# Kernel optimization log

Measured on AMD Instinct MI355X. Metric: run time of the kernel, lower is better.

The kernel has to match this reference:

```python
import jax, jax.numpy as jnp
import numpy as np
from jax import lax

B, H, W, C, NH = 16, 56, 56, 192, 6
L = H * W
DH = C // NH            # 32
HID = 4 * C             # 768
ETA = 1.0 / DH          # TTT inner-loop learning rate
EPS = 1e-5

# ---- RoPE rotation tables (deterministic buffer, shape (H, W, C//2)) ----
_kmax = C // 4
_theta = 1.0 / (10000.0 ** (np.arange(_kmax) / _kmax))
_ii, _jj = np.meshgrid(np.arange(H), np.arange(W), indexing='ij')
_ang = np.concatenate([_ii[..., None] * _theta, _jj[..., None] * _theta], axis=-1)  # (H,W,C/2)
_COS = jnp.asarray(np.cos(_ang), dtype=jnp.float32)
_SIN = jnp.asarray(np.sin(_ang), dtype=jnp.float32)


def layernorm(x, g, b):
    mu = jnp.mean(x, axis=-1, keepdims=True)
    var = jnp.mean(jnp.square(x - mu), axis=-1, keepdims=True)
    return (x - mu) * lax.rsqrt(var + EPS) * g + b


def dwconv3x3(x_blc, w, b):
    # x: (B, L, Ch) -> depthwise 3x3 conv over (H, W) -> (B, L, Ch)
    Ch = x_blc.shape[-1]
    xi = x_blc.reshape(B, H, W, Ch).transpose(0, 3, 1, 2)  # NCHW
    y = lax.conv_general_dilated(xi, w, (1, 1), 'SAME', feature_group_count=Ch,
                                 dimension_numbers=('NCHW', 'OIHW', 'NCHW'))
    y = y + b[None, :, None, None]
    return y.transpose(0, 2, 3, 1).reshape(B, L, Ch)


def rope(x):
    # x: (B, L, C); rotate complex pairs with 2D axial angles
    xr = x.reshape(B, H, W, C // 2, 2)
    re, im = xr[..., 0], xr[..., 1]
    o_re = _COS * re - _SIN * im
    o_im = _SIN * re + _COS * im
    return jnp.stack([o_re, o_im], axis=-1).reshape(B, L, C)


def ttt_attn(xn, qkv_w, qkv_b, W0, proj_w, proj_b):
    qkv = xn @ qkv_w.T + qkv_b                      # (B, L, 3C)
    q, k, v = jnp.split(qkv, 3, axis=-1)
    q = rope(q) * (DH ** -0.5)
    k = rope(k)

    def to_heads(t):  # (B,L,C) -> (L, B*NH, DH)
        return t.reshape(B, L, NH, DH).transpose(1, 0, 2, 3).reshape(L, B * NH, DH)
    qs, ks, vs = to_heads(q), to_heads(k), to_heads(v)

    Wst0 = jnp.broadcast_to(W0[None], (B, NH, DH, DH)).reshape(B * NH, DH, DH)

    def step(Wst, qkv_t):
        qt, kt, vt = qkv_t
        pred = jnp.einsum('bij,bj->bi', Wst, kt)
        Wn = Wst - ETA * (pred - vt)[:, :, None] * kt[:, None, :]
        ot = jnp.einsum('bij,bj->bi', Wn, qt)
        return Wn, ot

    _, out = lax.scan(step, Wst0, (qs, ks, vs))     # out: (L, B*NH, DH)
    out = out.reshape(L, B, NH, DH).transpose(1, 0, 2, 3).reshape(B, L, C)
    return out @ proj_w.T + proj_b


def setup_inputs() -> dict:
    key = jax.random.key(0)
    ks = jax.random.split(key, 12)
    s = 0.02
    return {
        'x': jax.random.normal(ks[0], (B, L, C), jnp.float32),
        'cpe_w': jax.random.normal(ks[1], (C, 1, 3, 3), jnp.float32) * s,
        'cpe_b': jnp.zeros((C,), jnp.float32),
        'n1_g': jnp.ones((C,), jnp.float32),
        'n1_b': jnp.zeros((C,), jnp.float32),
        'qkv_w': jax.random.normal(ks[2], (3 * C, C), jnp.float32) * s,
        'qkv_b': jnp.zeros((3 * C,), jnp.float32),
        'W0': jax.random.normal(ks[3], (NH, DH, DH), jnp.float32) * s,
        'proj_w': jax.random.normal(ks[4], (C, C), jnp.float32) * s,
        'proj_b': jnp.zeros((C,), jnp.float32),
        'n2_g': jnp.ones((C,), jnp.float32),
        'n2_b': jnp.zeros((C,), jnp.float32),
        'fc1_w': jax.random.normal(ks[5], (HID, C), jnp.float32) * s,
        'fc1_b': jnp.zeros((HID,), jnp.float32),
        'dwc_w': jax.random.normal(ks[6], (HID, 1, 3, 3), jnp.float32) * s,
        'dwc_b': jnp.zeros((HID,), jnp.float32),
        'fc2_w': jax.random.normal(ks[7], (C, HID), jnp.float32) * s,
        'fc2_b': jnp.zeros((C,), jnp.float32),
    }


def reference(x, cpe_w, cpe_b, n1_g, n1_b, qkv_w, qkv_b, W0, proj_w, proj_b,
              n2_g, n2_b, fc1_w, fc1_b, dwc_w, dwc_b, fc2_w, fc2_b):
    # CPE: conditional positional encoding (depthwise conv residual)
    x = x + dwconv3x3(x, cpe_w, cpe_b)
    # TTT attention branch
    x = x + ttt_attn(layernorm(x, n1_g, n1_b), qkv_w, qkv_b, W0, proj_w, proj_b)
    # MLP branch with depthwise conv
    h1 = jax.nn.gelu(layernorm(x, n2_g, n2_b) @ fc1_w.T + fc1_b, approximate=False)
    h1 = jax.nn.gelu(h1 + dwconv3x3(h1, dwc_w, dwc_b), approximate=False)
    x = x + (h1 @ fc2_w.T + fc2_b)
    return x
```

## Files before the change

### kernel.cpp

```cpp
#include <hip/hip_runtime.h>
#include <hip/hip_bf16.h>

#define Bc 16
#define Hc 56
#define Wcc 56
#define Cc 192
#define NHc 6
#define Lc 3136
#define DHc 32
#define HIDc 768
#define NHEAD 96
#define Sc 32
#define NCHUNK 98
#define NPAIR (NHEAD*NCHUNK)
#define ROWS (Bc*Lc)
#define GR2 (ROWS/2)
#define ETAc (1.0f/32.0f)

typedef unsigned short u16;
typedef unsigned int u32;
typedef __attribute__((ext_vector_type(8))) short bf16x8;
typedef __attribute__((ext_vector_type(4))) float f32x4;
typedef __attribute__((ext_vector_type(16))) float f32x16;

__device__ __forceinline__ float b2f(u16 v){ u32 u = ((u32)v)<<16; float f; __builtin_memcpy(&f,&u,4); return f; }
__device__ __forceinline__ u16 f2b(float f){ u32 u; __builtin_memcpy(&u,&f,4); u32 r = u + 0x7FFFu + ((u>>16)&1u); return (u16)(r>>16); }
__device__ __forceinline__ f32x16 zero16(){ f32x16 z = {0,0,0,0,0,0,0,0,0,0,0,0,0,0,0,0}; return z; }

__device__ __forceinline__ void make_bfrags(const f32x16& t, int hi, bf16x8& b1, bf16x8& b2){
  u32 P[8], S[8];
  #pragma unroll
  for (int q=0;q<4;q++){
    #pragma unroll
    for (int j=0;j<2;j++){
      u32 r; float lo = t[4*q+2*j], hv = t[4*q+2*j+1];
      asm("v_cvt_pk_bf16_f32 %0, %1, %2" : "=v"(r) : "v"(lo), "v"(hv));
      P[2*q+j] = r;
    }
  }
  #pragma unroll
  for (int i=0;i<8;i++) S[i] = (u32)__shfl_xor((int)P[i], 32);
  union { u32 u[4]; bf16x8 v; } f1, f2;
  if (hi==0){ f1.u[0]=P[0]; f1.u[1]=P[1]; f1.u[2]=S[0]; f1.u[3]=S[1];
              f2.u[0]=P[4]; f2.u[1]=P[5]; f2.u[2]=S[4]; f2.u[3]=S[5]; }
  else      { f1.u[0]=S[2]; f1.u[1]=S[3]; f1.u[2]=P[2]; f1.u[3]=P[3];
              f2.u[0]=S[6]; f2.u[1]=S[7]; f2.u[2]=P[6]; f2.u[3]=P[7]; }
  b1 = f1.v; b2 = f2.v;
}

__global__ __launch_bounds__(256) void cast_bf16_kernel(const float* __restrict__ src, u16* __restrict__ dst, int n){
  int i = blockIdx.x*256 + threadIdx.x;
  if (i < n) dst[i] = f2b(src[i]);
}

__global__ __launch_bounds__(256) void dwt_kernel(const float* __restrict__ w, float* __restrict__ wt, int CH){
  int i = blockIdx.x*256 + threadIdx.x;
  if (i < CH*9){ int ch = i/9, t = i - ch*9; wt[t*CH + ch] = w[i]; }
}

__global__ __launch_bounds__(256) void rope_tab_kernel(float* __restrict__ ct, float* __restrict__ st){
  int i = blockIdx.x*256 + threadIdx.x;
  int l = i/96, p = i - l*96;
  int h = l/Wcc, w = l - h*Wcc;
  int kk = (p<48)? p : p-48;
  float th = powf(10000.f, -(float)kk/48.f);
  float ang = (float)((p<48)? h : w) * th;
  ct[i] = cosf(ang);
  st[i] = sinf(ang);
}

__global__ __launch_bounds__(256) void cpe_kernel(const float* __restrict__ x, const float* __restrict__ cwt9,
                                                  const float* __restrict__ bs, u16* __restrict__ x1){
  int gid = blockIdx.x*256 + threadIdx.x;
  int cg = gid % 24; int row = gid / 24; int ch0 = cg*8;
  int l = row % Lc; int h = l/Wcc, w = l - h*Wcc;
  const float* xp = x + (size_t)row*Cc + ch0;
  float acc[8];
  { f32x4 b0 = *(const f32x4*)(bs+ch0), b1v = *(const f32x4*)(bs+ch0+4);
    acc[0]=b0[0];acc[1]=b0[1];acc[2]=b0[2];acc[3]=b0[3];
    acc[4]=b1v[0];acc[5]=b1v[1];acc[6]=b1v[2];acc[7]=b1v[3]; }
  #pragma unroll
  for (int kh=0;kh<3;kh++){
    int hh = h+kh-1; if (hh<0 || hh>=Hc) continue;
    #pragma unroll
    for (int kw=0;kw<3;kw++){
      int ww = w+kw-1; if (ww<0 || ww>=Wcc) continue;
      const float* ip = xp + ((kh-1)*Wcc + (kw-1))*Cc;
      f32x4 i0 = *(const f32x4*)ip, i1 = *(const f32x4*)(ip+4);
      const float* wp = cwt9 + (kh*3+kw)*Cc + ch0;
      f32x4 w0 = *(const f32x4*)wp, w1 = *(const f32x4*)(wp+4);
      acc[0] += i0[0]*w0[0]; acc[1] += i0[1]*w0[1]; acc[2] += i0[2]*w0[2]; acc[3] += i0[3]*w0[3];
      acc[4] += i1[0]*w1[0]; acc[5] += i1[1]*w1[1]; acc[6] += i1[2]*w1[2]; acc[7] += i1[3]*w1[3];
    }
  }
  f32x4 c0 = *(const f32x4*)xp, c1 = *(const f32x4*)(xp+4);
  union { bf16x8 v; u16 s[8]; } ov;
  ov.s[0]=f2b(c0[0]+acc[0]); ov.s[1]=f2b(c0[1]+acc[1]); ov.s[2]=f2b(c0[2]+acc[2]); ov.s[3]=f2b(c0[3]+acc[3]);
  ov.s[4]=f2b(c1[0]+acc[4]); ov.s[5]=f2b(c1[1]+acc[5]); ov.s[6]=f2b(c1[2]+acc[6]); ov.s[7]=f2b(c1[3]+acc[7]);
  *(bf16x8*)(x1 + (size_t)row*Cc + ch0) = ov.v;
}

template<int INF32>
__global__ __launch_bounds__(256) void ln_kernel(const u16* __restrict__ xb, const float* __restrict__ xf,
                                                 const float* __restrict__ g, const float* __restrict__ b,
                                                 u16* __restrict__ out){
  int row = blockIdx.x*4 + (threadIdx.x>>6);
  int lane = threadIdx.x & 63;
  float v0, v1, v2;
  if (INF32){
    const float* xr = xf + (size_t)row*Cc;
    v0 = xr[lane]; v1 = xr[lane+64]; v2 = xr[lane+128];
  } else {
    const u16* xr = xb + (size_t)row*Cc;
    v0 = b2f(xr[lane]); v1 = b2f(xr[lane+64]); v2 = b2f(xr[lane+128]);
  }
  float s = v0+v1+v2;
  float q = v0*v0 + v1*v1 + v2*v2;
  #pragma unroll
  for (int off=32; off; off>>=1){ s += __shfl_xor(s, off); q += __shfl_xor(q, off); }
  float mu = s*(1.f/Cc);
  float var = q*(1.f/Cc) - mu*mu;
  float rs = rsqrtf(var + 1e-5f);
  u16* orow = out + (size_t)row*Cc;
  orow[lane]     = f2b((v0-mu)*rs*g[lane]     + b[lane]);
  orow[lane+64]  = f2b((v1-mu)*rs*g[lane+64]  + b[lane+64]);
  orow[lane+128] = f2b((v2-mu)*rs*g[lane+128] + b[lane+128]);
}

template<int MODE, int BLKM, int KT>
__global__ __launch_bounds__(256) void gemm_kernel(
    const u16* __restrict__ A, const u16* __restrict__ Wt,
    const float* __restrict__ bias,
    float* __restrict__ outf, u16* __restrict__ outb,
    u16* __restrict__ vdst, const u16* __restrict__ residb, const float* __restrict__ residf)
{
  constexpr int WROWS = BLKM/2;
  constexpr int NF = WROWS/16;
  constexpr int NCH = KT/192;
  constexpr int NG = BLKM*192/(256*8);
  __shared__ u16 As[BLKM*200];
  int tid = threadIdx.x;
  int wid = tid>>6, lane = tid&63;
  int wr = wid>>1, wc = wid&1;
  int m0 = blockIdx.x*BLKM;
  int n0 = blockIdx.y*192 + wc*96;
  int ar = lane&15, kg = lane>>4;
  f32x4 acc[NF][6];
  #pragma unroll
  for (int f=0;f<NF;f++)
    #pragma unroll
    for (int c=0;c<6;c++){ f32x4 z = {0.f,0.f,0.f,0.f}; acc[f][c] = z; }
  bf16x8 bcur[6], bnxt[6];
  #pragma unroll
  for (int c=0;c<6;c++) bcur[c] = *(const bf16x8*)(Wt + (size_t)(n0 + c*16 + ar)*KT + kg*8);
  #pragma unroll
  for (int ch=0; ch<NCH; ch++){
    if (ch>0) __syncthreads();
    #pragma unroll
    for (int j=0;j<NG;j++){
      int g = j*256 + tid;
      int grow = g/24, gcol = (g - grow*24)*8;
      bf16x8 v = *(const bf16x8*)(A + (size_t)(m0+grow)*KT + ch*192 + gcol);
      *(bf16x8*)(As + grow*200 + gcol) = v;
    }
    __syncthreads();
    #pragma unroll
    for (int kc=0;kc<6;kc++){
      int s = ch*6 + kc;
      if (s+1 < NCH*6){
        int koff = ((s+1)/6)*192 + ((s+1)%6)*32 + kg*8;
        #pragma unroll
        for (int c=0;c<6;c++) bnxt[c] = *(const bf16x8*)(Wt + (size_t)(n0 + c*16 + ar)*KT + koff);
      }
      bf16x8 af[NF];
      #pragma unroll
      for (int f=0;f<NF;f++)
        af[f] = *(const bf16x8*)(As + (wr*WROWS + f*16 + ar)*200 + kc*32 + kg*8);
      #pragma unroll
      for (int f=0;f<NF;f++)
        #pragma unroll
        for (int c=0;c<6;c++)
          acc[f][c] = __builtin_amdgcn_mfma_f32_16x16x32_bf16(af[f], bcur[c], acc[f][c], 0,0,0);
      #pragma unroll
      for (int c=0;c<6;c++) bcur[c] = bnxt[c];
    }
  }
  int rb = kg*4;
  #pragma unroll
  for (int f=0;f<NF;f++){
    #pragma unroll
    for (int c=0;c<6;c++){
      int col = n0 + c*16 + ar;
      float bv = bias[col];
      #pragma unroll
      for (int j=0;j<4;j++){
        int row = m0 + wr*WROWS + f*16 + rb + j;
        float v = acc[f][c][j] + bv;
        if (MODE==0){
          if (col < 384) outb[(size_t)row*384 + col] = f2b(v);
          else {
            int bb = row/Lc; int l = row - bb*Lc;
            int nh = (col-384)>>5; int d = col&31;
            vdst[(((size_t)(bb*NHc+nh))*Lc + l)*DHc + d] = f2b(v);
          }
        } else if (MODE==1){
          outf[(size_t)row*Cc + col] = v + b2f(residb[(size_t)row*Cc + col]);
        } else if (MODE==2){
          float gv = 0.5f*v*(1.f + erff(v*0.70710678118654752f));
          outb[(size_t)row*HIDc + col] = f2b(gv);
        } else {
          outf[(size_t)row*Cc + col] = v + residf[(size_t)row*Cc + col];
        }
      }
    }
  }
}

__global__ __launch_bounds__(256) void rope_kernel(const u16* __restrict__ qk, const float* __restrict__ ct,
                                                   const float* __restrict__ st, u16* __restrict__ q_s, u16* __restrict__ k_s){
  int gid = blockIdx.x*256 + threadIdx.x;
  int sub = gid % 24; int row = gid / 24;
  int bb = row / Lc; int l = row - bb*Lc;
  bool isq = sub < 12; int pg = isq ? sub : sub-12;
  int p0 = pg*8;
  int cbase = (isq ? 0 : 192) + 2*p0;
  const u16* qr = qk + (size_t)row*384 + cbase;
  bf16x8 in0 = *(const bf16x8*)qr;
  bf16x8 in1 = *(const bf16x8*)(qr + 8);
  const float* cp = ct + l*96 + p0;
  const float* sp = st + l*96 + p0;
  f32x4 c0 = *(const f32x4*)cp, c1 = *(const f32x4*)(cp+4);
  f32x4 s0 = *(const f32x4*)sp, s1 = *(const f32x4*)(sp+4);
  float cs[8] = {c0[0],c0[1],c0[2],c0[3],c1[0],c1[1],c1[2],c1[3]};
  float sn[8] = {s0[0],s0[1],s0[2],s0[3],s1[0],s1[1],s1[2],s1[3]};
  float sc = isq ? 0.1767766952966369f : 1.0f;
  union { bf16x8 v; u16 s[8]; } o0, o1;
  #pragma unroll
  for (int j=0;j<4;j++){
    float re = b2f((u16)in0[2*j]), im = b2f((u16)in0[2*j+1]);
    o0.s[2*j]   = f2b((cs[j]*re - sn[j]*im)*sc);
    o0.s[2*j+1] = f2b((sn[j]*re + cs[j]*im)*sc);
  }
  #pragma unroll
  for (int j=0;j<4;j++){
    float re = b2f((u16)in1[2*j]), im = b2f((u16)in1[2*j+1]);
    o1.s[2*j]   = f2b((cs[4+j]*re - sn[4+j]*im)*sc);
    o1.s[2*j+1] = f2b((sn[4+j]*re + cs[4+j]*im)*sc);
  }
  int nh = pg>>1, d0 = (pg&1)*16;
  u16* dst = (isq ? q_s : k_s) + (((size_t)(bb*NHc+nh))*Lc + l)*DHc + d0;
  *(bf16x8*)dst = o0.v;
  *(bf16x8*)(dst+8) = o1.v;
}

__global__ __launch_bounds__(64) void ttta_kernel(const u16* __restrict__ k_s, const u16* __restrict__ v_s,
                                                  u16* __restrict__ u_s, u16* __restrict__ rn_s,
                                                  u16* __restrict__ af_s, u16* __restrict__ bc_s){
  __shared__ float Gl[1024];
  __shared__ u16 LK[32*40];
  __shared__ float LU[32*33];
  __shared__ float LR[32*33];
  int pair = blockIdx.x;
  int head = pair / NCHUNK;
  int l0 = (pair - head*NCHUNK) * Sc;
  int lane = threadIdx.x; int rr = lane&31; int hi = lane>>5; int ks = hi*8;
  const u16* kb = k_s + ((size_t)head*Lc + l0)*DHc;
  bf16x8 a0 = *(const bf16x8*)(kb + rr*32 + ks);
  bf16x8 a1 = *(const bf16x8*)(kb + rr*32 + 16 + ks);
  *(bf16x8*)(LK + rr*40 + ks) = a0;
  *(bf16x8*)(LK + rr*40 + 16 + ks) = a1;
  f32x16 g = zero16();
  g = __builtin_amdgcn_mfma_f32_32x32x16_bf16(a0, a0, g, 0,0,0);
  g = __builtin_amdgcn_mfma_f32_32x32x16_bf16(a1, a1, g, 0,0,0);
  #pragma unroll
  for (int reg=0;reg<16;reg++){
    int i = (reg&3) + 8*(reg>>2) + 4*hi;
    Gl[i*32 + rr] = ETAc * g[reg];
  }
  __syncthreads();
  float X[32];
  if (lane < 32){
    #pragma unroll
    for (int i=0;i<32;i++) X[i] = ETAc * b2f(v_s[((size_t)head*Lc + l0 + i)*DHc + lane]);
  } else {
    int m = lane-32;
    #pragma unroll
    for (int i=0;i<32;i++) X[i] = ETAc * b2f(kb[i*32 + m]);
  }
  #pragma unroll
  for (int i=1;i<32;i++){
    float a = X[i];
    #pragma unroll
    for (int j=0;j<i;j++) a -= Gl[i*32+j]*X[j];
    X[i] = a;
  }
  if (lane < 32){
    u16* dst = u_s + (size_t)pair*1024 + lane;
    #pragma unroll
    for (int i=0;i<32;i++) dst[i*32] = f2b(X[i]);
    #pragma unroll
    for (int i=0;i<32;i++) LU[lane*33 + i] = X[i];
  } else {
    u16* dst = rn_s + (size_t)pair*1024 + (lane&31);
    #pragma unroll
    for (int i=0;i<32;i++) dst[i*32] = f2b(-X[i]);
    #pragma unroll
    for (int i=0;i<32;i++) LR[(lane&31)*33 + i] = X[i];
  }
  __syncthreads();
  union { bf16x8 v; u16 s[8]; } kc1, kc2, uc1, uc2, rc1, rc2;
  #pragma unroll
  for (int s=0;s<8;s++){
    kc1.s[s] = LK[(ks+s)*40 + rr];
    kc2.s[s] = LK[(16+ks+s)*40 + rr];
    uc1.s[s] = f2b(LU[rr*33 + ks+s]);
    uc2.s[s] = f2b(LU[rr*33 + 16+ks+s]);
    rc1.s[s] = f2b(LR[rr*33 + ks+s]);
    rc2.s[s] = f2b(LR[rr*33 + 16+ks+s]);
  }
  f32x16 bacc = zero16();
  bacc = __builtin_amdgcn_mfma_f32_32x32x16_bf16(kc1.v, uc1.v, bacc, 0,0,0);
  bacc = __builtin_amdgcn_mfma_f32_32x32x16_bf16(kc2.v, uc2.v, bacc, 0,0,0);
  union { bf16x8 v; u16 s[8]; } bo1, bo2;
  #pragma unroll
  for (int r=0;r<8;r++){ bo1.s[r] = f2b(bacc[r]); bo2.s[r] = f2b(bacc[8+r]); }
  *(bf16x8*)(bc_s + (size_t)pair*1024 + lane*16) = bo1.v;
  *(bf16x8*)(bc_s + (size_t)pair*1024 + lane*16 + 8) = bo2.v;
  f32x16 aacc = zero16();
  aacc = __builtin_amdgcn_mfma_f32_32x32x16_bf16(rc1.v, kc1.v, aacc, 0,0,0);
  aacc = __builtin_amdgcn_mfma_f32_32x32x16_bf16(rc2.v, kc2.v, aacc, 0,0,0);
  f32x16 an;
  #pragma unroll
  for (int r=0;r<16;r++) an[r] = -aacc[r];
  bf16x8 f1, f2;
  make_bfrags(an, hi, f1, f2);
  *(bf16x8*)(af_s + (size_t)pair*1024 + lane*16) = f1;
  *(bf16x8*)(af_s + (size_t)pair*1024 + lane*16 + 8) = f2;
}

__global__ __launch_bounds__(64) void tttb_kernel(const u16* __restrict__ af_s, const u16* __restrict__ bc_s,
                                                  const float* __restrict__ W0, u16* __restrict__ w_snap){
  int head = blockIdx.x; int nh = head % NHc;
  int lane = threadIdx.x; int rr = lane&31; int hi = lane>>5;
  f32x16 T;
  const float* w0r = W0 + nh*1024 + rr*32 + 4*hi;
  #pragma unroll
  for (int q=0;q<4;q++){
    f32x4 v = *(const f32x4*)(w0r + 8*q);
    T[4*q+0]=v[0]; T[4*q+1]=v[1]; T[4*q+2]=v[2]; T[4*q+3]=v[3];
  }
  size_t hb = (size_t)head*NCHUNK;
  const bf16x8* afp = (const bf16x8*)(af_s + hb*1024);
  const bf16x8* bcp = (const bf16x8*)(bc_s + hb*1024);
  bf16x8 A1 = afp[lane*2], A2 = afp[lane*2+1];
  bf16x8 Bv1 = bcp[lane*2], Bv2 = bcp[lane*2+1];
  bf16x8 b1, b2;
  make_bfrags(T, hi, b1, b2);
  for (int c=0;c<NCHUNK;c++){
    bf16x8 nA1=A1, nA2=A2, nB1=Bv1, nB2=Bv2;
    if (c+1 < NCHUNK){
      int base = (c+1)*128 + lane*2;
      nA1 = afp[base]; nA2 = afp[base+1];
      nB1 = bcp[base]; nB2 = bcp[base+1];
    }
    u16* wrow = w_snap + (hb + c)*1024 + rr*32;
    *(bf16x8*)(wrow + hi*8) = b1;
    *(bf16x8*)(wrow + 16 + hi*8) = b2;
    f32x16 acc;
    #pragma unroll
    for (int r=0;r<8;r++){ acc[r] = T[r] + b2f((u16)Bv1[r]); acc[8+r] = T[8+r] + b2f((u16)Bv2[r]); }
    acc = __builtin_amdgcn_mfma_f32_32x32x16_bf16(A1, b1, acc, 0,0,0);
    acc = __builtin_amdgcn_mfma_f32_32x32x16_bf16(A2, b2, acc, 0,0,0);
    T = acc;
    make_bfrags(T, hi, b1, b2);
    A1=nA1; A2=nA2; Bv1=nB1; Bv2=nB2;
  }
}

__global__ __launch_bounds__(64) void tttc_kernel(const u16* __restrict__ q_s, const u16* __restrict__ k_s,
                                                  const u16* __restrict__ w_snap, const u16* __restrict__ u_s,
                                                  const u16* __restrict__ rn_s, u16* __restrict__ o_bf){
  __shared__ __align__(16) u16 Pl[32*40];
  int pair = blockIdx.x;
  int head = pair / NCHUNK;
  int ch = pair - head*NCHUNK;
  int l0 = ch*Sc;
  int lane = threadIdx.x; int rr = lane&31; int hi = lane>>5; int ks = hi*8;
  const u16* qb = q_s + ((size_t)head*Lc + l0)*DHc;
  const u16* kb = k_s + ((size_t)head*Lc + l0)*DHc;
  bf16x8 q0 = *(const bf16x8*)(qb + rr*32 + ks);
  bf16x8 q1 = *(const bf16x8*)(qb + rr*32 + 16 + ks);
  bf16x8 k0 = *(const bf16x8*)(kb + rr*32 + ks);
  bf16x8 k1 = *(const bf16x8*)(kb + rr*32 + 16 + ks);
  f32x16 p = zero16();
  p = __builtin_amdgcn_mfma_f32_32x32x16_bf16(q0, k0, p, 0,0,0);
  p = __builtin_amdgcn_mfma_f32_32x32x16_bf16(q1, k1, p, 0,0,0);
  #pragma unroll
  for (int reg=0;reg<16;reg++){
    int i = (reg&3)+8*(reg>>2)+4*hi;
    Pl[i*40+rr] = (rr<=i) ? f2b(p[reg]) : (u16)0;
  }
  const u16* wsb = w_snap + (size_t)pair*1024;
  bf16x8 tb0 = *(const bf16x8*)(wsb + rr*32 + ks);
  bf16x8 tb1 = *(const bf16x8*)(wsb + rr*32 + 16 + ks);
  const u16* ub = u_s + (size_t)pair*1024;
  f32x16 wr;
  #pragma unroll
  for (int r=0;r<16;r++){
    int i = (r&3)+8*(r>>2)+4*hi;
    wr[r] = b2f(ub[i*32 + rr]);
  }
  const u16* rb = rn_s + (size_t)pair*1024;
  bf16x8 rn0 = *(const bf16x8*)(rb + rr*32 + ks);
  bf16x8 rn1 = *(const bf16x8*)(rb + rr*32 + 16 + ks);
  wr = __builtin_amdgcn_mfma_f32_32x32x16_bf16(rn0, tb0, wr, 0,0,0);
  wr = __builtin_amdgcn_mfma_f32_32x32x16_bf16(rn1, tb1, wr, 0,0,0);
  bf16x8 wb0, wb1;
  make_bfrags(wr, hi, wb0, wb1);
  __syncthreads();
  f32x16 o = zero16();
  o = __builtin_amdgcn_mfma_f32_32x32x16_bf16(q0, tb0, o, 0,0,0);
  o = __builtin_amdgcn_mfma_f32_32x32x16_bf16(q1, tb1, o, 0,0,0);
  bf16x8 pa0 = *(const bf16x8*)(Pl + rr*40 + ks);
  bf16x8 pa1 = *(const bf16x8*)(Pl + rr*40 + 16 + ks);
  o = __builtin_amdgcn_mfma_f32_32x32x16_bf16(pa0, wb0, o, 0,0,0);
  o = __builtin_amdgcn_mfma_f32_32x32x16_bf16(pa1, wb1, o, 0,0,0);
  int bb = head/NHc, nh = head - bb*NHc;
  #pragma unroll
  for (int reg=0;reg<16;reg++){
    int i = (reg&3)+8*(reg>>2)+4*hi;
    o_bf[((size_t)(bb*Lc + l0 + i))*Cc + nh*32 + rr] = f2b(o[reg]);
  }
}

__global__ __launch_bounds__(256) void dwc_kernel(const u16* __restrict__ h1, const float* __restrict__ wt9,
                                                  const float* __restrict__ bs, u16* __restrict__ h2, int row0){
  int gid = blockIdx.x*256 + threadIdx.x;
  int cg = gid % 96; int lrow = gid / 96; int ch0 = cg*8;
  int row = row0 + lrow;
  int l = row % Lc; int h = l/Wcc, w = l - h*Wcc;
  const u16* hp = h1 + (size_t)lrow*HIDc + ch0;
  float acc[8];
  { f32x4 b0 = *(const f32x4*)(bs+ch0), b1v = *(const f32x4*)(bs+ch0+4);
    acc[0]=b0[0];acc[1]=b0[1];acc[2]=b0[2];acc[3]=b0[3];
    acc[4]=b1v[0];acc[5]=b1v[1];acc[6]=b1v[2];acc[7]=b1v[3]; }
  #pragma unroll
  for (int kh=0;kh<3;kh++){
    int hh = h+kh-1; if (hh<0 || hh>=Hc) continue;
    #pragma unroll
    for (int kw=0;kw<3;kw++){
      int ww = w+kw-1; if (ww<0 || ww>=Wcc) continue;
      bf16x8 iv = *(const bf16x8*)(hp + ((kh-1)*Wcc + (kw-1))*HIDc);
      const float* wp = wt9 + (kh*3+kw)*HIDc + ch0;
      f32x4 w0 = *(const f32x4*)wp, w1 = *(const f32x4*)(wp+4);
      acc[0] += b2f((u16)iv[0])*w0[0]; acc[1] += b2f((u16)iv[1])*w0[1];
      acc[2] += b2f((u16)iv[2])*w0[2]; acc[3] += b2f((u16)iv[3])*w0[3];
      acc[4] += b2f((u16)iv[4])*w1[0]; acc[5] += b2f((u16)iv[5])*w1[1];
      acc[6] += b2f((u16)iv[6])*w1[2]; acc[7] += b2f((u16)iv[7])*w1[3];
    }
  }
  bf16x8 cv = *(const bf16x8*)hp;
  union { bf16x8 v; u16 s[8]; } ov;
  #pragma unroll
  for (int j=0;j<8;j++){
    float v = b2f((u16)cv[j]) + acc[j];
    ov.s[j] = f2b(0.5f*v*(1.f + erff(v*0.70710678118654752f)));
  }
  *(bf16x8*)(h2 + (size_t)lrow*HIDc + ch0) = ov.v;
}

extern "C" void kernel_launch(void* const* d_in, const int* in_sizes, int n_in,
                              void* d_out, int out_size, void* d_ws, size_t ws_size,
                              hipStream_t stream){
  const float* x     = (const float*)d_in[0];
  const float* cpe_w = (const float*)d_in[1];
  const float* cpe_b = (const float*)d_in[2];
  const float* n1_g  = (const float*)d_in[3];
  const float* n1_b  = (const float*)d_in[4];
  const float* qkv_w = (const float*)d_in[5];
  const float* qkv_b = (const float*)d_in[6];
  const float* W0    = (const float*)d_in[7];
  const float* proj_w= (const float*)d_in[8];
  const float* proj_b= (const float*)d_in[9];
  const float* n2_g  = (const float*)d_in[10];
  const float* n2_b  = (const float*)d_in[11];
  const float* fc1_w = (const float*)d_in[12];
  const float* fc1_b = (const float*)d_in[13];
  const float* dwc_w = (const float*)d_in[14];
  const float* dwc_b = (const float*)d_in[15];
  const float* fc2_w = (const float*)d_in[16];
  const float* fc2_b = (const float*)d_in[17];

  char* ws = (char*)d_ws;
  size_t off = 0;
  auto alloc = [&](size_t bytes)->char*{
    char* p = ws + off;
    off += (bytes + 255) & ~(size_t)255;
    return p;
  };
  u16* wbqkv = (u16*)alloc((size_t)576*192*2);
  u16* wbproj= (u16*)alloc((size_t)192*192*2);
  u16* wbfc1 = (u16*)alloc((size_t)768*192*2);
  u16* wbfc2 = (u16*)alloc((size_t)192*768*2);
  float* dwt9 = (float*)alloc((size_t)9*HIDc*4);
  float* cwt9 = (float*)alloc((size_t)9*Cc*4);
  float* ctab = (float*)alloc((size_t)Lc*96*4);
  float* stab = (float*)alloc((size_t)Lc*96*4);
  u16* regA = (u16*)alloc((size_t)ROWS*Cc*2);
  u16* regB = (u16*)alloc((size_t)ROWS*Cc*2);
  u16* regD = (u16*)alloc((size_t)NHEAD*Lc*DHc*2);
  u16* regE = (u16*)alloc((size_t)NHEAD*Lc*DHc*2);
  u16* rn_s = (u16*)alloc((size_t)NPAIR*1024*2);
  u16* af_s = (u16*)alloc((size_t)NPAIR*1024*2);
  u16* wsn  = (u16*)alloc((size_t)NPAIR*1024*2);
  u16* qk = (u16*)d_out;
  u16* us = (u16*)d_out;
  u16* bc = us + (size_t)NPAIR*1024;
  float* x2 = (float*)d_out;

  u16* x1 = regA;
  u16* xn = regB;
  u16* qs = regB;
  u16* xn2 = regB;
  u16* vs = regD;
  u16* obf = regD;
  u16* ksb = regE;
  u16* h1 = regD;
  u16* h2 = rn_s;

  cast_bf16_kernel<<<(576*192+255)/256,256,0,stream>>>(qkv_w, wbqkv, 576*192);
  cast_bf16_kernel<<<(192*192+255)/256,256,0,stream>>>(proj_w, wbproj, 192*192);
  cast_bf16_kernel<<<(768*192+255)/256,256,0,stream>>>(fc1_w, wbfc1, 768*192);
  cast_bf16_kernel<<<(192*768+255)/256,256,0,stream>>>(fc2_w, wbfc2, 192*768);
  dwt_kernel<<<(768*9+255)/256,256,0,stream>>>(dwc_w, dwt9, HIDc);
  dwt_kernel<<<(192*9+255)/256,256,0,stream>>>(cpe_w, cwt9, Cc);
  rope_tab_kernel<<<(Lc*96)/256,256,0,stream>>>(ctab, stab);

  cpe_kernel<<<(ROWS*24)/256,256,0,stream>>>(x, cwt9, cpe_b, x1);
  ln_kernel<0><<<ROWS/4,256,0,stream>>>(x1, nullptr, n1_g, n1_b, xn);
  { dim3 g(ROWS/128, 3); gemm_kernel<0,128,192><<<g,256,0,stream>>>(xn, wbqkv, qkv_b, nullptr, qk, vs, nullptr, nullptr); }
  rope_kernel<<<(ROWS*24)/256,256,0,stream>>>(qk, ctab, stab, qs, ksb);
  ttta_kernel<<<NPAIR,64,0,stream>>>(ksb, vs, us, rn_s, af_s, bc);
  tttb_kernel<<<NHEAD,64,0,stream>>>(af_s, bc, W0, wsn);
  tttc_kernel<<<NPAIR,64,0,stream>>>(qs, ksb, wsn, us, rn_s, obf);
  { dim3 g(ROWS/128, 1); gemm_kernel<1,128,192><<<g,256,0,stream>>>(obf, wbproj, proj_b, x2, nullptr, nullptr, x1, nullptr); }
  ln_kernel<1><<<ROWS/4,256,0,stream>>>(nullptr, x2, n2_g, n2_b, xn2);
  for (int g4=0; g4<2; g4++){
    const u16* a_in = xn2 + (size_t)g4*GR2*Cc;
    float* xo = x2 + (size_t)g4*GR2*Cc;
    { dim3 g(GR2/128, 4); gemm_kernel<2,128,192><<<g,256,0,stream>>>(a_in, wbfc1, fc1_b, nullptr, h1, nullptr, nullptr, nullptr); }
    dwc_kernel<<<(GR2*96)/256,256,0,stream>>>(h1, dwt9, dwc_b, h2, g4*GR2);
    { dim3 g(GR2/64, 1); gemm_kernel<3,64,768><<<g,256,0,stream>>>(h2, wbfc2, fc2_b, xo, nullptr, nullptr, nullptr, xo); }
  }
}
```

Baseline: 553.6 us.

## Stage GEMM epilogues through LDS for coalesced vector stores and shrink row tile

```diff
diff --git a/kernel.cpp b/kernel.cpp
--- a/kernel.cpp
+++ b/kernel.cpp
@@ -127,27 +127,28 @@
   orow[lane+128] = f2b((v2-mu)*rs*g[lane+128] + b[lane+128]);
 }
 
-template<int MODE, int BLKM, int KT>
+template<int MODE, int KT>
 __global__ __launch_bounds__(256) void gemm_kernel(
     const u16* __restrict__ A, const u16* __restrict__ Wt,
     const float* __restrict__ bias,
     float* __restrict__ outf, u16* __restrict__ outb,
     u16* __restrict__ vdst, const u16* __restrict__ residb, const float* __restrict__ residf)
 {
-  constexpr int WROWS = BLKM/2;
-  constexpr int NF = WROWS/16;
   constexpr int NCH = KT/192;
-  constexpr int NG = BLKM*192/(256*8);
-  __shared__ u16 As[BLKM*200];
+  __shared__ __align__(16) char smem[64*200*2];
+  u16* As = (u16*)smem;
+  float* Os32 = (float*)smem;
+  u16* Osu = (u16*)smem;
   int tid = threadIdx.x;
   int wid = tid>>6, lane = tid&63;
   int wr = wid>>1, wc = wid&1;
-  int m0 = blockIdx.x*BLKM;
-  int n0 = blockIdx.y*192 + wc*96;
+  int m0 = blockIdx.x*64;
+  int nblk = blockIdx.y*192;
+  int n0 = nblk + wc*96;
   int ar = lane&15, kg = lane>>4;
-  f32x4 acc[NF][6];
-  #pragma unroll
-  for (int f=0;f<NF;f++)
+  f32x4 acc[2][6];
+  #pragma unroll
+  for (int f=0;f<2;f++)
     #pragma unroll
     for (int c=0;c<6;c++){ f32x4 z = {0.f,0.f,0.f,0.f}; acc[f][c] = z; }
   bf16x8 bcur[6], bnxt[6];
@@ -157,7 +158,7 @@
   for (int ch=0; ch<NCH; ch++){
     if (ch>0) __syncthreads();
     #pragma unroll
-    for (int j=0;j<NG;j++){
+    for (int j=0;j<6;j++){
       int g = j*256 + tid;
       int grow = g/24, gcol = (g - grow*24)*8;
       bf16x8 v = *(const bf16x8*)(A + (size_t)(m0+grow)*KT + ch*192 + gcol);
@@ -172,12 +173,12 @@
         #pragma unroll
         for (int c=0;c<6;c++) bnxt[c] = *(const bf16x8*)(Wt + (size_t)(n0 + c*16 + ar)*KT + koff);
       }
-      bf16x8 af[NF];
+      bf16x8 af[2];
       #pragma unroll
-      for (int f=0;f<NF;f++)
-        af[f] = *(const bf16x8*)(As + (wr*WROWS + f*16 + ar)*200 + kc*32 + kg*8);
+      for (int f=0;f<2;f++)
+        af[f] = *(const bf16x8*)(As + (wr*32 + f*16 + ar)*200 + kc*32 + kg*8);
       #pragma unroll
-      for (int f=0;f<NF;f++)
+      for (int f=0;f<2;f++)
         #pragma unroll
         for (int c=0;c<6;c++)
           acc[f][c] = __builtin_amdgcn_mfma_f32_16x16x32_bf16(af[f], bcur[c], acc[f][c], 0,0,0);
@@ -185,33 +186,70 @@
       for (int c=0;c<6;c++) bcur[c] = bnxt[c];
     }
   }
-  int rb = kg*4;
-  #pragma unroll
-  for (int f=0;f<NF;f++){
-    #pragma unroll
-    for (int c=0;c<6;c++){
-      int col = n0 + c*16 + ar;
-      float bv = bias[col];
+  __syncthreads();
+  if (MODE==0 || MODE==2){
+    #pragma unroll
+    for (int f=0;f<2;f++){
       #pragma unroll
-      for (int j=0;j<4;j++){
-        int row = m0 + wr*WROWS + f*16 + rb + j;
-        float v = acc[f][c][j] + bv;
-        if (MODE==0){
-          if (col < 384) outb[(size_t)row*384 + col] = f2b(v);
-          else {
-            int bb = row/Lc; int l = row - bb*Lc;
-            int nh = (col-384)>>5; int d = col&31;
-            vdst[(((size_t)(bb*NHc+nh))*Lc + l)*DHc + d] = f2b(v);
-          }
-        } else if (MODE==1){
-          outf[(size_t)row*Cc + col] = v + b2f(residb[(size_t)row*Cc + col]);
-        } else if (MODE==2){
-          float gv = 0.5f*v*(1.f + erff(v*0.70710678118654752f));
-          outb[(size_t)row*HIDc + col] = f2b(gv);
-        } else {
-          outf[(size_t)row*Cc + col] = v + residf[(size_t)row*Cc + col];
+      for (int c=0;c<6;c++){
+        float bv = bias[n0 + c*16 + ar];
+        #pragma unroll
+        for (int j=0;j<4;j++){
+          float v = acc[f][c][j] + bv;
+          if (MODE==2) v = 0.5f*v*(1.f + erff(v*0.70710678118654752f));
+          Osu[(wr*32 + f*16 + kg*4 + j)*200 + wc*96 + c*16 + ar] = f2b(v);
         }
       }
+    }
+    __syncthreads();
+    #pragma unroll
+    for (int j=0;j<6;j++){
+      int g = j*256 + tid;
+      int grow = g/24, gcol = (g - grow*24)*8;
+      bf16x8 v = *(const bf16x8*)(Osu + grow*200 + gcol);
+      int row = m0 + grow, col = nblk + gcol;
+      if (MODE==2){
+        *(bf16x8*)(outb + (size_t)row*HIDc + col) = v;
+      } else if (col < 384){
+        *(bf16x8*)(outb + (size_t)row*384 + col) = v;
+      } else {
+        int bb = row/Lc; int l = row - bb*Lc;
+        int nh = gcol>>5, d = gcol&31;
+        *(bf16x8*)(vdst + (((size_t)(bb*NHc+nh))*Lc + l)*DHc + d) = v;
+      }
+    }
+  } else {
+    #pragma unroll
+    for (int half=0; half<2; half++){
+      if (wc==half){
+        #pragma unroll
+        for (int f=0;f<2;f++){
+          #pragma unroll
+          for (int c=0;c<6;c++){
+            float bv = bias[n0 + c*16 + ar];
+            #pragma unroll
+            for (int j=0;j<4;j++)
+              Os32[(wr*32 + f*16 + kg*4 + j)*100 + c*16 + ar] = acc[f][c][j] + bv;
+          }
+        }
+      }
+      __syncthreads();
+      #pragma unroll
+      for (int j=0;j<6;j++){
+        int g = j*256 + tid;
+        int grow = g/24, qcol = (g - grow*24)*4;
+        f32x4 v = *(const f32x4*)(Os32 + grow*100 + qcol);
+        int row = m0 + grow, colg = half*96 + qcol;
+        if (MODE==1){
+          const u16* rp = residb + (size_t)row*Cc + colg;
+          v[0] += b2f(rp[0]); v[1] += b2f(rp[1]); v[2] += b2f(rp[2]); v[3] += b2f(rp[3]);
+        } else {
+          f32x4 rv = *(const f32x4*)(residf + (size_t)row*Cc + colg);
+          v[0] += rv[0]; v[1] += rv[1]; v[2] += rv[2]; v[3] += rv[3];
+        }
+        *(f32x4*)(outf + (size_t)row*Cc + colg) = v;
+      }
+      if (half==0) __syncthreads();
     }
   }
 }
@@ -538,18 +576,18 @@
 
   cpe_kernel<<<(ROWS*24)/256,256,0,stream>>>(x, cwt9, cpe_b, x1);
   ln_kernel<0><<<ROWS/4,256,0,stream>>>(x1, nullptr, n1_g, n1_b, xn);
-  { dim3 g(ROWS/128, 3); gemm_kernel<0,128,192><<<g,256,0,stream>>>(xn, wbqkv, qkv_b, nullptr, qk, vs, nullptr, nullptr); }
+  { dim3 g(ROWS/64, 3); gemm_kernel<0,192><<<g,256,0,stream>>>(xn, wbqkv, qkv_b, nullptr, qk, vs, nullptr, nullptr); }
   rope_kernel<<<(ROWS*24)/256,256,0,stream>>>(qk, ctab, stab, qs, ksb);
   ttta_kernel<<<NPAIR,64,0,stream>>>(ksb, vs, us, rn_s, af_s, bc);
   tttb_kernel<<<NHEAD,64,0,stream>>>(af_s, bc, W0, wsn);
   tttc_kernel<<<NPAIR,64,0,stream>>>(qs, ksb, wsn, us, rn_s, obf);
-  { dim3 g(ROWS/128, 1); gemm_kernel<1,128,192><<<g,256,0,stream>>>(obf, wbproj, proj_b, x2, nullptr, nullptr, x1, nullptr); }
+  { dim3 g(ROWS/64, 1); gemm_kernel<1,192><<<g,256,0,stream>>>(obf, wbproj, proj_b, x2, nullptr, nullptr, x1, nullptr); }
   ln_kernel<1><<<ROWS/4,256,0,stream>>>(nullptr, x2, n2_g, n2_b, xn2);
   for (int g4=0; g4<2; g4++){
     const u16* a_in = xn2 + (size_t)g4*GR2*Cc;
     float* xo = x2 + (size_t)g4*GR2*Cc;
-    { dim3 g(GR2/128, 4); gemm_kernel<2,128,192><<<g,256,0,stream>>>(a_in, wbfc1, fc1_b, nullptr, h1, nullptr, nullptr, nullptr); }
+    { dim3 g(GR2/64, 4); gemm_kernel<2,192><<<g,256,0,stream>>>(a_in, wbfc1, fc1_b, nullptr, h1, nullptr, nullptr, nullptr); }
     dwc_kernel<<<(GR2*96)/256,256,0,stream>>>(h1, dwt9, dwc_b, h2, g4*GR2);
-    { dim3 g(GR2/64, 1); gemm_kernel<3,64,768><<<g,256,0,stream>>>(h2, wbfc2, fc2_b, xo, nullptr, nullptr, nullptr, xo); }
-  }
-}
+    { dim3 g(GR2/64, 1); gemm_kernel<3,768><<<g,256,0,stream>>>(h2, wbfc2, fc2_b, xo, nullptr, nullptr, nullptr, xo); }
+  }
+}
```

Result: faster. 526.2 us (-4.9%).
